# Kernel optimization log

Hardware: AMD Instinct MI355X
Metric: run time of the kernel (lower is better)

The kernel has to match this reference:

```python
import jax, jax.numpy as jnp
import numpy as np
from functools import partial

T, B, IN, H, OUT = 512, 64, 512, 1024, 512


def _qrnn_layer(x, W, b):
    """One QRNN layer (window=1, fo-pool). x: (T,B,D) -> (T,B,H)."""
    g = jnp.einsum('tbd,dh->tbh', x, W) + b        # (T,B,3H)
    z, f, o = jnp.split(g, 3, axis=-1)
    z = jnp.tanh(z)
    f = jax.nn.sigmoid(f)
    o = jax.nn.sigmoid(o)

    def step(c, zf):
        z_t, f_t = zf
        c = f_t * c + (1.0 - f_t) * z_t            # fo-pool recurrence
        return c, c

    c0 = jnp.zeros((x.shape[1], W.shape[1] // 3), x.dtype)
    _, cs = jax.lax.scan(step, c0, (z, f))         # cs: (T,B,H)
    return o * cs


def setup_inputs() -> dict:
    key = jax.random.key(0)
    ks = jax.random.split(key, 5)
    scale = lambda fan_in: 1.0 / np.sqrt(fan_in)
    return {
        'x':   jax.random.normal(ks[0], (T, B, IN), jnp.float32),
        'W0':  jax.random.normal(ks[1], (IN, 3 * H), jnp.float32) * scale(IN),
        'b0':  jnp.zeros((3 * H,), jnp.float32),
        'W1':  jax.random.normal(ks[2], (H, 3 * H), jnp.float32) * scale(H),
        'b1':  jnp.zeros((3 * H,), jnp.float32),
        'Wfc': jax.random.normal(ks[3], (H, OUT), jnp.float32) * scale(H),
        'bfc': jnp.zeros((OUT,), jnp.float32),
    }


def reference(x, W0, b0, W1, b1, Wfc, bfc):
    h = _qrnn_layer(x, W0, b0)                     # layer 0: (T,B,H)
    h = _qrnn_layer(h, W1, b1)                     # layer 1: (T,B,H)
    out = jnp.einsum('tbh,ho->tbo', h, Wfc) + bfc  # fc over all timesteps
    return out
```

## Files before the change

### kernel.cpp

```cpp
#include <hip/hip_runtime.h>
#include <hip/hip_bf16.h>


#define QT 512
#define QB 64
#define QIN 512
#define QH 1024
#define QOUT 512
#define QM (QT * QB)
#define SEG 32
#define SL (QT / SEG)

typedef unsigned short ushort_t;
typedef __attribute__((ext_vector_type(8))) short bf16x8;
typedef __attribute__((ext_vector_type(4))) float f32x4;

__device__ __forceinline__ float u2f(ushort_t u) {
    union { unsigned int i; float f; } v;
    v.i = ((unsigned int)u) << 16;
    return v.f;
}

__device__ __forceinline__ ushort_t f2bf(float f) {
    union { float f; unsigned int i; } v;
    v.f = f;
    unsigned int r = v.i + 0x7fffu + ((v.i >> 16) & 1u);
    return (ushort_t)(r >> 16);
}

__device__ __forceinline__ void glds16(const ushort_t* g, ushort_t* l) {
    __builtin_amdgcn_global_load_lds(
        (const __attribute__((address_space(1))) void*)g,
        (__attribute__((address_space(3))) void*)l, 16, 0, 0);
}

__global__ __launch_bounds__(256) void cvt_bf16(const float* __restrict__ src,
                                                ushort_t* __restrict__ dst) {
    const int i = blockIdx.x * 256 + threadIdx.x;
    float4 v = ((const float4*)src)[i];
    ushort4 o;
    o.x = f2bf(v.x); o.y = f2bf(v.y); o.z = f2bf(v.z); o.w = f2bf(v.w);
    ((ushort4*)dst)[i] = o;
}

__global__ __launch_bounds__(256) void transpose_cvt(
    const float* __restrict__ W, ushort_t* __restrict__ WT, int K, int N) {
    __shared__ float t[32][33];
    const int tx = threadIdx.x & 31, ty = threadIdx.x >> 5;
    const int n0 = blockIdx.x * 32, k0 = blockIdx.y * 32;
#pragma unroll
    for (int i = 0; i < 4; ++i)
        t[ty + 8 * i][tx] = W[(size_t)(k0 + ty + 8 * i) * N + n0 + tx];
    __syncthreads();
#pragma unroll
    for (int i = 0; i < 4; ++i)
        WT[(size_t)(n0 + ty + 8 * i) * K + k0 + tx] = f2bf(t[tx][ty + 8 * i]);
}

template <int MODE>
__global__ __launch_bounds__(256) void gemm_mfma(
    const ushort_t* __restrict__ A, const ushort_t* __restrict__ BT,
    const float* __restrict__ bias, void* __restrict__ out,
    int K, int c0, int CW) {
    __shared__ ushort_t As[128 * 64];
    __shared__ ushort_t Bs[128 * 64];

    const int tid = threadIdx.x;
    const int lane = tid & 63;
    const int w = tid >> 6;
    const int wr = w >> 1, wc = w & 1;
    const int m0 = blockIdx.y * 128;

    int nW, nOut, outstride, gate = 0;
    if (MODE == 0) {
        const int per = CW >> 7;
        gate = blockIdx.x / per;
        const int nloc = (blockIdx.x - gate * per) * 128;
        nW = gate * QH + c0 + nloc;
        nOut = gate * CW + nloc;
        outstride = 3 * CW;
    } else {
        nW = blockIdx.x * 128;
        nOut = nW;
        outstride = QOUT;
    }

    size_t aoff[4], boff[4];
    int soff[4];
#pragma unroll
    for (int j = 0; j < 4; ++j) {
        const int s = ((w * 4 + j) << 6) + lane;
        const int ms = s >> 3;
        const int kg = (s & 7) ^ (ms & 7);
        aoff[j] = (size_t)(m0 + ms) * K + kg * 8;
        boff[j] = (size_t)(nW + ms) * K + kg * 8;
        soff[j] = (w * 4 + j) << 9;
    }

    const int fl = lane & 15, fq = lane >> 4, l7 = lane & 7;
    int aidx[2][4], bidx[2][4];
#pragma unroll
    for (int ks = 0; ks < 2; ++ks)
#pragma unroll
        for (int i = 0; i < 4; ++i) {
            const int am = wr * 64 + i * 16 + fl;
            const int bn = wc * 64 + i * 16 + fl;
            const int kq = ks * 4 + fq;
            aidx[ks][i] = (am * 8 + (kq ^ l7)) * 8;
            bidx[ks][i] = (bn * 8 + (kq ^ l7)) * 8;
        }

    f32x4 acc[4][4];
#pragma unroll
    for (int i = 0; i < 4; ++i)
#pragma unroll
        for (int j = 0; j < 4; ++j) acc[i][j] = {0.f, 0.f, 0.f, 0.f};

    for (int k0 = 0; k0 < K; k0 += 64) {
        __syncthreads();
#pragma unroll
        for (int j = 0; j < 4; ++j) glds16(A + aoff[j] + k0, &As[soff[j]]);
#pragma unroll
        for (int j = 0; j < 4; ++j) glds16(BT + boff[j] + k0, &Bs[soff[j]]);
        __syncthreads();
#pragma unroll
        for (int ks = 0; ks < 2; ++ks) {
            bf16x8 af[4], bv[4];
#pragma unroll
            for (int i = 0; i < 4; ++i)
                af[i] = *(const bf16x8*)&As[aidx[ks][i]];
#pragma unroll
            for (int j = 0; j < 4; ++j)
                bv[j] = *(const bf16x8*)&Bs[bidx[ks][j]];
#pragma unroll
            for (int i = 0; i < 4; ++i)
#pragma unroll
                for (int j = 0; j < 4; ++j)
                    acc[i][j] = __builtin_amdgcn_mfma_f32_16x16x32_bf16(
                        af[i], bv[j], acc[i][j], 0, 0, 0);
        }
    }

    const float ak = (gate == 0) ? 2.8853900817779268f : -1.4426950408889634f;
    const float aa = (gate == 0) ? -2.f : 1.f;
    const float ad = (gate == 0) ? 1.f : 0.f;

    const int rbase = fq * 4;
#pragma unroll
    for (int i = 0; i < 4; ++i) {
#pragma unroll
        for (int j = 0; j < 4; ++j) {
            const int col = nOut + wc * 64 + j * 16 + fl;
            const float bvv = bias[nW + wc * 64 + j * 16 + fl];
            const int row0 = m0 + wr * 64 + i * 16 + rbase;
#pragma unroll
            for (int r = 0; r < 4; ++r) {
                float v = acc[i][j][r] + bvv;
                if (MODE == 0) {
                    v = aa * __builtin_amdgcn_rcpf(
                                 1.f + __builtin_amdgcn_exp2f(ak * v)) +
                        ad;
                    ((ushort_t*)out)[(size_t)(row0 + r) * outstride + col] =
                        f2bf(v);
                } else {
                    ((float*)out)[(size_t)(row0 + r) * outstride + col] = v;
                }
            }
        }
    }
}


__global__ __launch_bounds__(256) void scan_p1(const ushort_t* __restrict__ g,
                                               float* __restrict__ Aseg,
                                               float* __restrict__ Bseg,
                                               int CW) {
    const int idx = blockIdx.x * 256 + threadIdx.x;
    const int hh = idx % CW;
    const int sb = idx / CW;
    const int b = sb % QB;
    const int s = sb / QB;
    const ushort_t* gp = g + ((size_t)(s * SL * QB + b) * 3) * CW + hh;
    const size_t grow = (size_t)QB * 3 * CW;
    float zv[SL], fv[SL];
#pragma unroll
    for (int t = 0; t < SL; ++t) {
        zv[t] = u2f(gp[0]);
        fv[t] = u2f(gp[CW]);
        gp += grow;
    }
    float A = 1.f, Bc = 0.f;
#pragma unroll
    for (int t = 0; t < SL; ++t) {
        Bc = fv[t] * Bc + (1.f - fv[t]) * zv[t];
        A *= fv[t];
    }
    Aseg[idx] = A;
    Bseg[idx] = Bc;
}

__global__ __launch_bounds__(256) void scan_p2(const float* __restrict__ Aseg,
                                               const float* __restrict__ Bseg,
                                               float* __restrict__ cstart,
                                               int CW) {
    const int idx = blockIdx.x * 256 + threadIdx.x;
    const size_t stride = (size_t)QB * CW;
    float Av[SEG], Bv[SEG];
#pragma unroll
    for (int s = 0; s < SEG; ++s) {
        Av[s] = Aseg[s * stride + idx];
        Bv[s] = Bseg[s * stride + idx];
    }
    float c = 0.f;
#pragma unroll
    for (int s = 0; s < SEG; ++s) {
        cstart[s * stride + idx] = c;
        c = Av[s] * c + Bv[s];
    }
}

__global__ __launch_bounds__(256) void scan_p3(const ushort_t* __restrict__ g,
                                               const float* __restrict__ cstart,
                                               ushort_t* __restrict__ h,
                                               int c0, int CW) {
    const int idx = blockIdx.x * 256 + threadIdx.x;
    const int hh = idx % CW;
    const int sb = idx / CW;
    const int b = sb % QB;
    const int s = sb / QB;
    const ushort_t* gp = g + ((size_t)(s * SL * QB + b) * 3) * CW + hh;
    ushort_t* hp = h + (size_t)(s * SL * QB + b) * QH + c0 + hh;
    const size_t grow = (size_t)QB * 3 * CW;
    const size_t hrow = (size_t)QB * QH;
    float zv[SL], fv[SL], ov[SL];
#pragma unroll
    for (int t = 0; t < SL; ++t) {
        zv[t] = u2f(gp[0]);
        fv[t] = u2f(gp[CW]);
        ov[t] = u2f(gp[2 * CW]);
        gp += grow;
    }
    float c = cstart[idx];
#pragma unroll
    for (int t = 0; t < SL; ++t) {
        c = fv[t] * c + (1.f - fv[t]) * zv[t];
        *hp = f2bf(ov[t] * c);
        hp += hrow;
    }
}

extern "C" void kernel_launch(void* const* d_in, const int* in_sizes, int n_in,
                              void* d_out, int out_size, void* d_ws,
                              size_t ws_size, hipStream_t stream) {
    const float* x   = (const float*)d_in[0];
    const float* W0  = (const float*)d_in[1];
    const float* b0  = (const float*)d_in[2];
    const float* W1  = (const float*)d_in[3];
    const float* b1  = (const float*)d_in[4];
    const float* Wfc = (const float*)d_in[5];
    const float* bfc = (const float*)d_in[6];
    float* out = (float*)d_out;

    char* p = (char*)d_ws;
    ushort_t* h0   = (ushort_t*)p;  p += (size_t)QM * QH * 2;
    ushort_t* h1   = (ushort_t*)p;
    ushort_t* x_bf = (ushort_t*)p;  p += (size_t)QM * QH * 2;
    ushort_t* W0T  = (ushort_t*)p;  p += (size_t)3 * QH * QIN * 2;
    ushort_t* W1T  = (ushort_t*)p;  p += (size_t)3 * QH * QH * 2;
    ushort_t* WfcT = (ushort_t*)p;  p += (size_t)QOUT * QH * 2;
    const size_t base = (size_t)(p - (char*)d_ws);

    int CW = QH;
    while (CW > 128 &&
           base + 3 * (size_t)QB * CW * SEG * 4 + (size_t)QM * 3 * CW * 2 >
               ws_size)
        CW >>= 1;
    const int nch = QH / CW;

    float* Aseg   = (float*)p;  p += (size_t)QB * CW * SEG * 4;
    float* Bseg   = (float*)p;  p += (size_t)QB * CW * SEG * 4;
    float* cstart = (float*)p;  p += (size_t)QB * CW * SEG * 4;
    ushort_t* g   = (ushort_t*)p;

    dim3 blk(256);

    cvt_bf16<<<dim3(QM * QIN / 1024), blk, 0, stream>>>(x, x_bf);
    transpose_cvt<<<dim3(3 * QH / 32, QIN / 32), blk, 0, stream>>>(
        W0, W0T, QIN, 3 * QH);
    transpose_cvt<<<dim3(3 * QH / 32, QH / 32), blk, 0, stream>>>(
        W1, W1T, QH, 3 * QH);
    transpose_cvt<<<dim3(QOUT / 32, QH / 32), blk, 0, stream>>>(
        Wfc, WfcT, QH, QOUT);

    const dim3 ggrid(3 * (CW >> 7), QM / 128);
    const dim3 p13grid(SEG * QB * CW / 256);
    const dim3 p2grid(QB * CW / 256);

    for (int ci = 0; ci < nch; ++ci) {
        gemm_mfma<0><<<ggrid, blk, 0, stream>>>(x_bf, W0T, b0, g, QIN,
                                                ci * CW, CW);
        scan_p1<<<p13grid, blk, 0, stream>>>(g, Aseg, Bseg, CW);
        scan_p2<<<p2grid, blk, 0, stream>>>(Aseg, Bseg, cstart, CW);
        scan_p3<<<p13grid, blk, 0, stream>>>(g, cstart, h0, ci * CW, CW);
    }
    for (int ci = 0; ci < nch; ++ci) {
        gemm_mfma<0><<<ggrid, blk, 0, stream>>>(h0, W1T, b1, g, QH,
                                                ci * CW, CW);
        scan_p1<<<p13grid, blk, 0, stream>>>(g, Aseg, Bseg, CW);
        scan_p2<<<p2grid, blk, 0, stream>>>(Aseg, Bseg, cstart, CW);
        scan_p3<<<p13grid, blk, 0, stream>>>(g, cstart, h1, ci * CW, CW);
    }
    gemm_mfma<1><<<dim3(QOUT / 128, QM / 128), blk, 0, stream>>>(
        h1, WfcT, bfc, out, QH, 0, 0);
}
```

Baseline: 774.7 us.

## Replace GEMM with 256x256-tile, 4-stage pipelined MFMA kernel with XCD-aware block remap

Replaces the 128x128-tile GEMM with a 512-thread kernel computing 256x256 output tiles. It streams K in 32-wide slices through a 4-deep LDS ring buffer using async global-to-LDS loads and explicit vmcnt waits, so one barrier per slice replaces two. It also swizzles block indices across 8 chiplets for L2 locality and raises wave priority around the MFMA bursts. The goal is to hide memory latency and improve data reuse, at the cost of larger LDS use (128KB), more accumulator registers, and a minimum chunk width of 256.

Result: no change. 786.1 us (+1.5%).

```diff
diff --git a/kernel.cpp b/kernel.cpp
--- a/kernel.cpp
+++ b/kernel.cpp
@@ -57,102 +57,123 @@
         WT[(size_t)(n0 + ty + 8 * i) * K + k0 + tx] = f2bf(t[tx][ty + 8 * i]);
 }
 
-template <int MODE>
-__global__ __launch_bounds__(256) void gemm_mfma(
+template <int MODE, int K>
+__global__ __launch_bounds__(512, 2) void gemm256(
     const ushort_t* __restrict__ A, const ushort_t* __restrict__ BT,
     const float* __restrict__ bias, void* __restrict__ out,
-    int K, int c0, int CW) {
-    __shared__ ushort_t As[128 * 64];
-    __shared__ ushort_t Bs[128 * 64];
+    int c0, int CW) {
+    constexpr int NT = K / 32;
+    __shared__ ushort_t As[4 * 8192];
+    __shared__ ushort_t Bs[4 * 8192];
 
     const int tid = threadIdx.x;
     const int lane = tid & 63;
     const int w = tid >> 6;
-    const int wr = w >> 1, wc = w & 1;
-    const int m0 = blockIdx.y * 128;
+    const int wr = w >> 2, wc = w & 3;
+
+    const int gx = gridDim.x;
+    const int nwg = gx * gridDim.y;
+    int flat = blockIdx.y * gx + blockIdx.x;
+    flat = (flat & 7) * (nwg >> 3) + (flat >> 3);
+    const int by = flat / gx;
+    const int bx = flat - by * gx;
+    const int m0 = by * 256;
 
     int nW, nOut, outstride, gate = 0;
     if (MODE == 0) {
-        const int per = CW >> 7;
-        gate = blockIdx.x / per;
-        const int nloc = (blockIdx.x - gate * per) * 128;
+        const int per = CW >> 8;
+        gate = bx / per;
+        const int nloc = (bx - gate * per) * 256;
         nW = gate * QH + c0 + nloc;
         nOut = gate * CW + nloc;
         outstride = 3 * CW;
     } else {
-        nW = blockIdx.x * 128;
+        nW = bx * 256;
         nOut = nW;
         outstride = QOUT;
     }
 
-    size_t aoff[4], boff[4];
-    int soff[4];
-#pragma unroll
-    for (int j = 0; j < 4; ++j) {
-        const int s = ((w * 4 + j) << 6) + lane;
-        const int ms = s >> 3;
-        const int kg = (s & 7) ^ (ms & 7);
-        aoff[j] = (size_t)(m0 + ms) * K + kg * 8;
-        boff[j] = (size_t)(nW + ms) * K + kg * 8;
-        soff[j] = (w * 4 + j) << 9;
-    }
-
-    const int fl = lane & 15, fq = lane >> 4, l7 = lane & 7;
-    int aidx[2][4], bidx[2][4];
-#pragma unroll
-    for (int ks = 0; ks < 2; ++ks)
-#pragma unroll
-        for (int i = 0; i < 4; ++i) {
-            const int am = wr * 64 + i * 16 + fl;
-            const int bn = wc * 64 + i * 16 + fl;
-            const int kq = ks * 4 + fq;
-            aidx[ks][i] = (am * 8 + (kq ^ l7)) * 8;
-            bidx[ks][i] = (bn * 8 + (kq ^ l7)) * 8;
+    size_t aoff[2], boff[2];
+    int ldso[2];
+#pragma unroll
+    for (int j = 0; j < 2; ++j) {
+        const int c = w * 128 + j * 64 + lane;
+        const int r = c >> 2;
+        const int gs = (c & 3) ^ ((r >> 1) & 3);
+        aoff[j] = (size_t)(m0 + r) * K + gs * 8;
+        boff[j] = (size_t)(nW + r) * K + gs * 8;
+        ldso[j] = w * 1024 + j * 512;
+    }
+
+    const int fl = lane & 15, fq = lane >> 4;
+    const int laneoff = fl * 32 + ((fq ^ ((fl >> 1) & 3)) << 3);
+
+    f32x4 acc[8][4];
+#pragma unroll
+    for (int i = 0; i < 8; ++i)
+#pragma unroll
+        for (int j = 0; j < 4; ++j) acc[i][j] = {0.f, 0.f, 0.f, 0.f};
+
+#pragma unroll
+    for (int t = 0; t < 3; ++t) {
+        const int slot = t * 8192;
+#pragma unroll
+        for (int j = 0; j < 2; ++j)
+            glds16(A + aoff[j] + t * 32, &As[slot + ldso[j]]);
+#pragma unroll
+        for (int j = 0; j < 2; ++j)
+            glds16(BT + boff[j] + t * 32, &Bs[slot + ldso[j]]);
+    }
+    asm volatile("s_waitcnt vmcnt(8)" ::: "memory");
+    __builtin_amdgcn_s_barrier();
+
+    for (int kt = 0; kt < NT; ++kt) {
+        if (kt + 3 < NT) {
+            const int slot = ((kt + 3) & 3) * 8192;
+            const size_t kb = (size_t)(kt + 3) * 32;
+#pragma unroll
+            for (int j = 0; j < 2; ++j)
+                glds16(A + aoff[j] + kb, &As[slot + ldso[j]]);
+#pragma unroll
+            for (int j = 0; j < 2; ++j)
+                glds16(BT + boff[j] + kb, &Bs[slot + ldso[j]]);
         }
-
-    f32x4 acc[4][4];
-#pragma unroll
-    for (int i = 0; i < 4; ++i)
-#pragma unroll
-        for (int j = 0; j < 4; ++j) acc[i][j] = {0.f, 0.f, 0.f, 0.f};
-
-    for (int k0 = 0; k0 < K; k0 += 64) {
-        __syncthreads();
-#pragma unroll
-        for (int j = 0; j < 4; ++j) glds16(A + aoff[j] + k0, &As[soff[j]]);
-#pragma unroll
-        for (int j = 0; j < 4; ++j) glds16(BT + boff[j] + k0, &Bs[soff[j]]);
-        __syncthreads();
-#pragma unroll
-        for (int ks = 0; ks < 2; ++ks) {
-            bf16x8 af[4], bv[4];
-#pragma unroll
-            for (int i = 0; i < 4; ++i)
-                af[i] = *(const bf16x8*)&As[aidx[ks][i]];
+        const int sa = (kt & 3) * 8192 + wr * 4096 + laneoff;
+        const int sb = (kt & 3) * 8192 + wc * 2048 + laneoff;
+        bf16x8 af[8], bv[4];
+#pragma unroll
+        for (int i = 0; i < 8; ++i) af[i] = *(const bf16x8*)&As[sa + i * 512];
+#pragma unroll
+        for (int j = 0; j < 4; ++j) bv[j] = *(const bf16x8*)&Bs[sb + j * 512];
+        __builtin_amdgcn_s_setprio(1);
+#pragma unroll
+        for (int i = 0; i < 8; ++i)
 #pragma unroll
             for (int j = 0; j < 4; ++j)
-                bv[j] = *(const bf16x8*)&Bs[bidx[ks][j]];
-#pragma unroll
-            for (int i = 0; i < 4; ++i)
-#pragma unroll
-                for (int j = 0; j < 4; ++j)
-                    acc[i][j] = __builtin_amdgcn_mfma_f32_16x16x32_bf16(
-                        af[i], bv[j], acc[i][j], 0, 0, 0);
-        }
+                acc[i][j] = __builtin_amdgcn_mfma_f32_16x16x32_bf16(
+                    af[i], bv[j], acc[i][j], 0, 0, 0);
+        __builtin_amdgcn_s_setprio(0);
+        if (kt < NT - 3)
+            asm volatile("s_waitcnt vmcnt(8)" ::: "memory");
+        else if (kt == NT - 3)
+            asm volatile("s_waitcnt vmcnt(4)" ::: "memory");
+        else if (kt == NT - 2)
+            asm volatile("s_waitcnt vmcnt(0)" ::: "memory");
+        if (kt < NT - 1) __builtin_amdgcn_s_barrier();
     }
 
     const float ak = (gate == 0) ? 2.8853900817779268f : -1.4426950408889634f;
     const float aa = (gate == 0) ? -2.f : 1.f;
     const float ad = (gate == 0) ? 1.f : 0.f;
 
-    const int rbase = fq * 4;
-#pragma unroll
-    for (int i = 0; i < 4; ++i) {
-#pragma unroll
-        for (int j = 0; j < 4; ++j) {
-            const int col = nOut + wc * 64 + j * 16 + fl;
-            const float bvv = bias[nW + wc * 64 + j * 16 + fl];
-            const int row0 = m0 + wr * 64 + i * 16 + rbase;
+#pragma unroll
+    for (int j = 0; j < 4; ++j) {
+        const int cb = wc * 64 + j * 16 + fl;
+        const float bvv = bias[nW + cb];
+        const int col = nOut + cb;
+#pragma unroll
+        for (int i = 0; i < 8; ++i) {
+            const int row0 = m0 + wr * 128 + i * 16 + fq * 4;
 #pragma unroll
             for (int r = 0; r < 4; ++r) {
                 float v = acc[i][j][r] + bvv;
@@ -271,7 +292,7 @@
     const size_t base = (size_t)(p - (char*)d_ws);
 
     int CW = QH;
-    while (CW > 128 &&
+    while (CW > 256 &&
            base + 3 * (size_t)QB * CW * SEG * 4 + (size_t)QM * 3 * CW * 2 >
                ws_size)
         CW >>= 1;
@@ -283,6 +304,7 @@
     ushort_t* g   = (ushort_t*)p;
 
     dim3 blk(256);
+    dim3 blk5(512);
 
     cvt_bf16<<<dim3(QM * QIN / 1024), blk, 0, stream>>>(x, x_bf);
     transpose_cvt<<<dim3(3 * QH / 32, QIN / 32), blk, 0, stream>>>(
@@ -292,24 +314,24 @@
     transpose_cvt<<<dim3(QOUT / 32, QH / 32), blk, 0, stream>>>(
         Wfc, WfcT, QH, QOUT);
 
-    const dim3 ggrid(3 * (CW >> 7), QM / 128);
+    const dim3 ggrid(3 * (CW >> 8), QM / 256);
     const dim3 p13grid(SEG * QB * CW / 256);
     const dim3 p2grid(QB * CW / 256);
 
     for (int ci = 0; ci < nch; ++ci) {
-        gemm_mfma<0><<<ggrid, blk, 0, stream>>>(x_bf, W0T, b0, g, QIN,
-                                                ci * CW, CW);
+        gemm256<0, QIN><<<ggrid, blk5, 0, stream>>>(x_bf, W0T, b0, g,
+                                                    ci * CW, CW);
         scan_p1<<<p13grid, blk, 0, stream>>>(g, Aseg, Bseg, CW);
         scan_p2<<<p2grid, blk, 0, stream>>>(Aseg, Bseg, cstart, CW);
         scan_p3<<<p13grid, blk, 0, stream>>>(g, cstart, h0, ci * CW, CW);
     }
     for (int ci = 0; ci < nch; ++ci) {
-        gemm_mfma<0><<<ggrid, blk, 0, stream>>>(h0, W1T, b1, g, QH,
-                                                ci * CW, CW);
+        gemm256<0, QH><<<ggrid, blk5, 0, stream>>>(h0, W1T, b1, g,
+                                                   ci * CW, CW);
         scan_p1<<<p13grid, blk, 0, stream>>>(g, Aseg, Bseg, CW);
         scan_p2<<<p2grid, blk, 0, stream>>>(Aseg, Bseg, cstart, CW);
         scan_p3<<<p13grid, blk, 0, stream>>>(g, cstart, h1, ci * CW, CW);
     }
-    gemm_mfma<1><<<dim3(QOUT / 128, QM / 128), blk, 0, stream>>>(
-        h1, WfcT, bfc, out, QH, 0, 0);
-}
+    gemm256<1, QH><<<dim3(QOUT / 256, QM / 256), blk5, 0, stream>>>(
+        h1, WfcT, bfc, out, 0, 0);
+}
```
